# Kernel tuning notes

Measured on AMD Instinct MI355X. Metric: run time of the kernel, lower is better.

Reference implementation:

```python
import jax, jax.numpy as jnp
import numpy as np

B, S, D, F, E, NS, K = 2, 1024, 1024, 4096, 8, 8, 2
FS = F // NS  # shared-expert hidden size = d_ff // num_shared_experts


def setup_inputs() -> dict:
    key = jax.random.key(0)
    ks = jax.random.split(key, 8)
    scale = 0.02
    return {
        "hidden_states": jax.random.normal(ks[0], (B, S, D), jnp.float32),
        "gate_W": jax.random.normal(ks[1], (E, D), jnp.float32) * scale,
        "w1_e": jax.random.normal(ks[2], (E, D, F), jnp.float32) * scale,
        "w3_e": jax.random.normal(ks[3], (E, D, F), jnp.float32) * scale,
        "w2_e": jax.random.normal(ks[4], (E, F, D), jnp.float32) * scale,
        "w1_s": jax.random.normal(ks[5], (NS, D, FS), jnp.float32) * scale,
        "w3_s": jax.random.normal(ks[6], (NS, D, FS), jnp.float32) * scale,
        "w2_s": jax.random.normal(ks[7], (NS, FS, D), jnp.float32) * scale,
    }


def reference(hidden_states, gate_W, w1_e, w3_e, w2_e, w1_s, w3_s, w2_s):
    b, s, d = hidden_states.shape
    e = gate_W.shape[0]
    flat = hidden_states.reshape(-1, d)            # [T, D]
    T = flat.shape[0]

    # --- gate: softmax over experts, top-k probs scattered (k=0 slot only survives) ---
    logits = (flat @ gate_W.T).astype(jnp.float32)  # [T, E]
    probs = jax.nn.softmax(logits, axis=-1)
    top_v, top_i = jax.lax.top_k(probs, K)          # [T, K]
    gates = jnp.zeros((T, e), probs.dtype).at[jnp.arange(T)[:, None], top_i].set(top_v)

    # --- routed experts: module runs every expert densely on all tokens ---
    g = jax.nn.silu(jnp.einsum('td,edf->etf', flat, w1_e))  # [E, T, F]
    u = jnp.einsum('td,edf->etf', flat, w3_e)
    out_e = jnp.einsum('etf,efd->etd', g * u, w2_e)         # [E, T, D]
    routed = jnp.einsum('te,etd->td', gates, out_e).reshape(b, s, d)

    # --- shared experts (mean over NS experts) ---
    gs = jax.nn.silu(jnp.einsum('bsd,ndf->nbsf', hidden_states, w1_s))
    us = jnp.einsum('bsd,ndf->nbsf', hidden_states, w3_s)
    shared = jnp.einsum('nbsf,nfd->bsd', gs * us, w2_s) / w1_s.shape[0]

    alpha = 0.5
    return alpha * shared + (1.0 - alpha) * routed
```

## Files before the change

kernel.cpp:

```cpp
#include <hip/hip_runtime.h>

#define T 2048
#define D 1024
#define F 4096
#define E 8
#define NS 8
#define FS 512
#define SHB 5120
#define NROWS 7168
#define MT_MAX 56

typedef float floatx4 __attribute__((ext_vector_type(4)));
typedef short short8 __attribute__((ext_vector_type(8)));

__device__ __forceinline__ unsigned short f2bf(float f) {
  unsigned int u = __float_as_uint(f);
  u += 0x7FFF + ((u >> 16) & 1);
  return (unsigned short)(u >> 16);
}

__device__ __forceinline__ void glds16(const void* g, void* l) {
  __builtin_amdgcn_global_load_lds(
      (const __attribute__((address_space(1))) void*)g,
      (__attribute__((address_space(3))) void*)l, 16, 0, 0);
}

__global__ void gate_kernel(const float* __restrict__ x, const float* __restrict__ gW,
                            unsigned short* __restrict__ xb, int* __restrict__ cnt,
                            int* __restrict__ list_tok, float* __restrict__ list_gate) {
  int t = blockIdx.x, tid = threadIdx.x;
  const float* xr = x + (size_t)t * D;
  float acc[E];
#pragma unroll
  for (int e = 0; e < E; ++e) acc[e] = 0.f;
  for (int d = tid; d < D; d += 256) {
    float xv = xr[d];
    xb[(size_t)t * D + d] = f2bf(xv);
#pragma unroll
    for (int e = 0; e < E; ++e) acc[e] += xv * gW[e * D + d];
  }
#pragma unroll
  for (int o = 32; o > 0; o >>= 1)
#pragma unroll
    for (int e = 0; e < E; ++e) acc[e] += __shfl_down(acc[e], o, 64);
  __shared__ float wred[4][E];
  int lane = tid & 63, wv = tid >> 6;
  if (lane == 0)
#pragma unroll
    for (int e = 0; e < E; ++e) wred[wv][e] = acc[e];
  __syncthreads();
  if (tid == 0) {
    float l[E];
#pragma unroll
    for (int e = 0; e < E; ++e) l[e] = wred[0][e] + wred[1][e] + wred[2][e] + wred[3][e];
    int i1 = 0; float m1 = l[0];
    for (int e = 1; e < E; ++e) if (l[e] > m1) { m1 = l[e]; i1 = e; }
    int i2 = -1; float m2 = -3.4e38f;
    for (int e = 0; e < E; ++e) if (e != i1 && l[e] > m2) { m2 = l[e]; i2 = e; }
    float s = 0.f, p[E];
#pragma unroll
    for (int e = 0; e < E; ++e) { p[e] = __expf(l[e] - m1); s += p[e]; }
    float inv = 1.f / s;
    int p1 = atomicAdd(&cnt[i1], 1);
    list_tok[i1 * T + p1] = t; list_gate[i1 * T + p1] = p[i1] * inv;
    int p2 = atomicAdd(&cnt[i2], 1);
    list_tok[i2 * T + p2] = t; list_gate[i2 * T + p2] = p[i2] * inv;
  }
}

__global__ void offsets_kernel(const int* __restrict__ cnt, int* __restrict__ off,
                               int* __restrict__ mt_expert) {
  if (threadIdx.x == 0 && blockIdx.x == 0) {
    int o = 0;
    for (int e = 0; e < E; ++e) { off[e] = o; o += (cnt[e] + 127) & ~127; }
    off[E] = o;
    for (int i = 0; i < MT_MAX; ++i) mt_expert[i] = -1;
    for (int e = 0; e < E; ++e) {
      int t0 = off[e] >> 7, nt = (cnt[e] + 127) >> 7;
      for (int i = 0; i < nt; ++i) mt_expert[t0 + i] = e;
    }
    for (int i = SHB >> 7; i < MT_MAX; ++i) mt_expert[i] = E;
  }
}

__global__ void scatter_kernel(const int* __restrict__ cnt, const int* __restrict__ off,
                               const int* __restrict__ list_tok, const float* __restrict__ list_gate,
                               int* __restrict__ tok_of_row, float* __restrict__ row_scale,
                               int* __restrict__ tok_rows, int* __restrict__ tk) {
  int idx = blockIdx.x * 256 + threadIdx.x;
  int e = idx >> 11, i = idx & (T - 1);
  if (e < E && i < cnt[e]) {
    int row = off[e] + i;
    int t = list_tok[e * T + i];
    tok_of_row[row] = t;
    row_scale[row] = 0.5f * list_gate[e * T + i];
    int k = atomicAdd(&tk[t], 1);
    tok_rows[2 * t + k] = row;
  }
}

__global__ void transpose_cast(const float* __restrict__ in, unsigned short* __restrict__ out,
                               int R, int C) {
  in += (size_t)blockIdx.z * R * C;
  out += (size_t)blockIdx.z * R * C;
  int r0 = blockIdx.y * 32, c0 = blockIdx.x * 32;
  __shared__ float tile[32][33];
  int tid = threadIdx.x;
  {
    int rl = tid >> 3, cl = (tid & 7) * 4;
    float4 v = *(const float4*)(in + (size_t)(r0 + rl) * C + c0 + cl);
    tile[rl][cl] = v.x; tile[rl][cl + 1] = v.y;
    tile[rl][cl + 2] = v.z; tile[rl][cl + 3] = v.w;
  }
  __syncthreads();
  {
    int cl = tid >> 3, rq = (tid & 7) * 4;
    int c = c0 + cl, r = r0 + rq;
    ushort4 v;
    v.x = f2bf(tile[rq][cl]);     v.y = f2bf(tile[rq + 1][cl]);
    v.z = f2bf(tile[rq + 2][cl]); v.w = f2bf(tile[rq + 3][cl]);
    int Rt = R >> 5;
    size_t o = ((size_t)(c >> 7) * Rt + (r >> 5)) * 4096 + (size_t)(c & 127) * 32 + (r & 31);
    *(ushort4*)(out + o) = v;
  }
}

__global__ __launch_bounds__(256, 2) void up_gemm(
    const unsigned short* __restrict__ xb, const unsigned short* __restrict__ W1T,
    const unsigned short* __restrict__ W3T, const unsigned short* __restrict__ W1sT,
    const unsigned short* __restrict__ W3sT, const int* __restrict__ mt_expert,
    const int* __restrict__ tok_of_row, unsigned short* __restrict__ Hb) {
  int mt = blockIdx.y, ntile = blockIdx.x;
  int e = mt_expert[mt];
  if (e < 0) return;
  const unsigned short *B1, *B3;
  if (e < E) {
    B1 = W1T + (size_t)e * F * D;
    B3 = W3T + (size_t)e * F * D;
  } else {
    B1 = W1sT; B3 = W3sT;
  }
  __shared__ unsigned short Au0[128 * 32], B1u0[128 * 32], B3u0[128 * 32];
  __shared__ unsigned short Au1[128 * 32], B1u1[128 * 32], B3u1[128 * 32];
  __shared__ unsigned short Au2[128 * 32], B1u2[128 * 32], B3u2[128 * 32];
  int tid = threadIdx.x;
  int lane = tid & 63, wv = tid >> 6, wm = wv >> 1, wn = wv & 1;
  int row16 = lane & 15, quad = lane >> 4;
  int qsw8 = (quad ^ ((lane >> 1) & 3)) * 8;
  int swzb = (tid >> 2) * 64 + (((tid & 3) ^ ((tid >> 3) & 3)) * 16);
  int lw = wv * 1024;

  int r1 = tid >> 2;
  int hrow1 = mt * 128 + r1, hrow2 = hrow1 + 64;
  int srow1 = (e < E) ? tok_of_row[hrow1] : (hrow1 - SHB);
  int srow2 = (e < E) ? tok_of_row[hrow2] : (hrow2 - SHB);
  int asl = ((tid & 3) ^ ((tid >> 3) & 3)) * 16;
  const char* asrc1 = (const char*)(xb + (size_t)srow1 * D) + asl;
  const char* asrc2 = (const char*)(xb + (size_t)srow2 * D) + asl;
  const char* b1t = (const char*)(B1 + (size_t)ntile * (D / 32) * 4096);
  const char* b3t = (const char*)(B3 + (size_t)ntile * (D / 32) * 4096);

  floatx4 accg[4][4], accu[4][4];
#pragma unroll
  for (int i = 0; i < 4; ++i)
#pragma unroll
    for (int j = 0; j < 4; ++j) {
      accg[i][j] = (floatx4){0.f, 0.f, 0.f, 0.f};
      accu[i][j] = (floatx4){0.f, 0.f, 0.f, 0.f};
    }

  auto stage = [&](int kt, unsigned short* Ad, unsigned short* B1d, unsigned short* B3d) {
    size_t ko = (size_t)kt * 64;
    size_t bo = (size_t)kt * 8192;
    glds16(asrc1 + ko, (char*)Ad + lw);
    glds16(asrc2 + ko, (char*)Ad + 4096 + lw);
    glds16(b1t + bo + swzb, (char*)B1d + lw);
    glds16(b1t + bo + 4096 + swzb, (char*)B1d + 4096 + lw);
    glds16(b3t + bo + swzb, (char*)B3d + lw);
    glds16(b3t + bo + 4096 + swzb, (char*)B3d + 4096 + lw);
  };
  auto compute = [&](const unsigned short* Ac, const unsigned short* B1c,
                     const unsigned short* B3c) {
    short8 af[4], b1f[4], b3f[4];
#pragma unroll
    for (int mi = 0; mi < 4; ++mi)
      af[mi] = *(const short8*)(Ac + (wm * 64 + mi * 16 + row16) * 32 + qsw8);
#pragma unroll
    for (int ni = 0; ni < 4; ++ni) {
      b1f[ni] = *(const short8*)(B1c + (wn * 64 + ni * 16 + row16) * 32 + qsw8);
      b3f[ni] = *(const short8*)(B3c + (wn * 64 + ni * 16 + row16) * 32 + qsw8);
    }
#pragma unroll
    for (int mi = 0; mi < 4; ++mi)
#pragma unroll
      for (int ni = 0; ni < 4; ++ni) {
        accg[mi][ni] = __builtin_amdgcn_mfma_f32_16x16x32_bf16(af[mi], b1f[ni], accg[mi][ni], 0, 0, 0);
        accu[mi][ni] = __builtin_amdgcn_mfma_f32_16x16x32_bf16(af[mi], b3f[ni], accu[mi][ni], 0, 0, 0);
      }
  };

  stage(0, Au0, B1u0, B3u0);
  stage(1, Au1, B1u1, B3u1);
  asm volatile("s_waitcnt vmcnt(6)" ::: "memory");
  __builtin_amdgcn_s_barrier();
  for (int t = 0; t < 30; t += 3) {
    stage(t + 2, Au2, B1u2, B3u2);
    compute(Au0, B1u0, B3u0);
    asm volatile("s_waitcnt vmcnt(6)" ::: "memory");
    __builtin_amdgcn_s_barrier();
    stage(t + 3, Au0, B1u0, B3u0);
    compute(Au1, B1u1, B3u1);
    asm volatile("s_waitcnt vmcnt(6)" ::: "memory");
    __builtin_amdgcn_s_barrier();
    stage(t + 4, Au1, B1u1, B3u1);
    compute(Au2, B1u2, B3u2);
    asm volatile("s_waitcnt vmcnt(6)" ::: "memory");
    __builtin_amdgcn_s_barrier();
  }
  compute(Au0, B1u0, B3u0);
  asm volatile("s_waitcnt vmcnt(0)" ::: "memory");
  __builtin_amdgcn_s_barrier();
  compute(Au1, B1u1, B3u1);

#pragma unroll
  for (int mi = 0; mi < 4; ++mi)
#pragma unroll
    for (int ni = 0; ni < 4; ++ni)
#pragma unroll
      for (int r = 0; r < 4; ++r) {
        int hrow = mt * 128 + wm * 64 + mi * 16 + quad * 4 + r;
        int col = ntile * 128 + wn * 64 + ni * 16 + row16;
        float g = accg[mi][ni][r], u = accu[mi][ni][r];
        float h = g * u / (1.0f + __expf(-g));
        size_t o = ((size_t)(hrow >> 7) * 128 + (col >> 5)) * 4096 + (size_t)(hrow & 127) * 32 + (col & 31);
        Hb[o] = f2bf(h);
      }
}

__global__ __launch_bounds__(256, 2) void down_gemm(
    const unsigned short* __restrict__ Hb, const unsigned short* __restrict__ W2T,
    const unsigned short* __restrict__ W2sT, const int* __restrict__ mt_expert,
    const float* __restrict__ row_scale, float* __restrict__ O) {
  int mt = blockIdx.y, ntile = blockIdx.x, kz = blockIdx.z;
  int e = mt_expert[mt];
  if (e < 0) return;
  const char* Bt = (const char*)(((e < E) ? (W2T + (size_t)e * D * F) : W2sT)
                                 + (size_t)ntile * (F / 32) * 4096);
  const char* At = (const char*)(Hb + (size_t)mt * (F / 32) * 4096);
  O += (size_t)kz * NROWS * D;
  __shared__ unsigned short Ad0[128 * 32], Bd0[128 * 32];
  __shared__ unsigned short Ad1[128 * 32], Bd1[128 * 32];
  __shared__ unsigned short Ad2[128 * 32], Bd2[128 * 32];
  int tid = threadIdx.x;
  int lane = tid & 63, wv = tid >> 6, wm = wv >> 1, wn = wv & 1;
  int row16 = lane & 15, quad = lane >> 4;
  int qsw8 = (quad ^ ((lane >> 1) & 3)) * 8;
  int swzb = (tid >> 2) * 64 + (((tid & 3) ^ ((tid >> 3) & 3)) * 16);
  int lw = wv * 1024;
  floatx4 acc[4][4];
#pragma unroll
  for (int i = 0; i < 4; ++i)
#pragma unroll
    for (int j = 0; j < 4; ++j) acc[i][j] = (floatx4){0.f, 0.f, 0.f, 0.f};

  auto stage = [&](int kt, unsigned short* Ad, unsigned short* Bd) {
    size_t o = (size_t)kt * 8192;
    glds16(At + o + swzb, (char*)Ad + lw);
    glds16(At + o + 4096 + swzb, (char*)Ad + 4096 + lw);
    glds16(Bt + o + swzb, (char*)Bd + lw);
    glds16(Bt + o + 4096 + swzb, (char*)Bd + 4096 + lw);
  };
  auto compute = [&](const unsigned short* Ac, const unsigned short* Bc) {
    short8 af[4], bf[4];
#pragma unroll
    for (int mi = 0; mi < 4; ++mi)
      af[mi] = *(const short8*)(Ac + (wm * 64 + mi * 16 + row16) * 32 + qsw8);
#pragma unroll
    for (int ni = 0; ni < 4; ++ni)
      bf[ni] = *(const short8*)(Bc + (wn * 64 + ni * 16 + row16) * 32 + qsw8);
#pragma unroll
    for (int mi = 0; mi < 4; ++mi)
#pragma unroll
      for (int ni = 0; ni < 4; ++ni)
        acc[mi][ni] = __builtin_amdgcn_mfma_f32_16x16x32_bf16(af[mi], bf[ni], acc[mi][ni], 0, 0, 0);
  };

  int k0 = kz * 64;
  stage(k0 + 0, Ad0, Bd0);
  stage(k0 + 1, Ad1, Bd1);
  asm volatile("s_waitcnt vmcnt(4)" ::: "memory");
  __builtin_amdgcn_s_barrier();
  for (int t = 0; t < 60; t += 3) {
    stage(k0 + t + 2, Ad2, Bd2);
    compute(Ad0, Bd0);
    asm volatile("s_waitcnt vmcnt(4)" ::: "memory");
    __builtin_amdgcn_s_barrier();
    stage(k0 + t + 3, Ad0, Bd0);
    compute(Ad1, Bd1);
    asm volatile("s_waitcnt vmcnt(4)" ::: "memory");
    __builtin_amdgcn_s_barrier();
    stage(k0 + t + 4, Ad1, Bd1);
    compute(Ad2, Bd2);
    asm volatile("s_waitcnt vmcnt(4)" ::: "memory");
    __builtin_amdgcn_s_barrier();
  }
  stage(k0 + 62, Ad2, Bd2);
  compute(Ad0, Bd0);
  asm volatile("s_waitcnt vmcnt(4)" ::: "memory");
  __builtin_amdgcn_s_barrier();
  stage(k0 + 63, Ad0, Bd0);
  compute(Ad1, Bd1);
  asm volatile("s_waitcnt vmcnt(4)" ::: "memory");
  __builtin_amdgcn_s_barrier();
  compute(Ad2, Bd2);
  asm volatile("s_waitcnt vmcnt(0)" ::: "memory");
  __builtin_amdgcn_s_barrier();
  compute(Ad0, Bd0);

#pragma unroll
  for (int mi = 0; mi < 4; ++mi)
#pragma unroll
    for (int ni = 0; ni < 4; ++ni)
#pragma unroll
      for (int r = 0; r < 4; ++r) {
        int grow = mt * 128 + wm * 64 + mi * 16 + quad * 4 + r;
        int col = ntile * 128 + wn * 64 + ni * 16 + row16;
        float scale = (grow < SHB) ? row_scale[grow] : 0.0625f;
        O[(size_t)grow * D + col] = acc[mi][ni][r] * scale;
      }
}

__global__ void combine_kernel(const float* __restrict__ O, const int* __restrict__ tok_rows,
                               float* __restrict__ out) {
  int idx = blockIdx.x * 256 + threadIdx.x;
  int t = idx >> 8, c = idx & 255;
  int r0 = tok_rows[2 * t], r1 = tok_rows[2 * t + 1];
  const float4* O4 = (const float4*)O;
  const size_t HLF = (size_t)NROWS * 256;
  float4 a = O4[(size_t)r0 * 256 + c];
  float4 b = O4[(size_t)r1 * 256 + c];
  float4 s = O4[((size_t)SHB + t) * 256 + c];
  float4 a2 = O4[HLF + (size_t)r0 * 256 + c];
  float4 b2 = O4[HLF + (size_t)r1 * 256 + c];
  float4 s2 = O4[HLF + ((size_t)SHB + t) * 256 + c];
  float4 r;
  r.x = a.x + b.x + s.x + a2.x + b2.x + s2.x;
  r.y = a.y + b.y + s.y + a2.y + b2.y + s2.y;
  r.z = a.z + b.z + s.z + a2.z + b2.z + s2.z;
  r.w = a.w + b.w + s.w + a2.w + b2.w + s2.w;
  ((float4*)out)[idx] = r;
}

extern "C" void kernel_launch(void* const* d_in, const int* in_sizes, int n_in,
                              void* d_out, int out_size, void* d_ws, size_t ws_size,
                              hipStream_t stream) {
  (void)in_sizes; (void)n_in; (void)out_size; (void)ws_size;
  const float* x   = (const float*)d_in[0];
  const float* gW  = (const float*)d_in[1];
  const float* w1e = (const float*)d_in[2];
  const float* w3e = (const float*)d_in[3];
  const float* w2e = (const float*)d_in[4];
  const float* w1s = (const float*)d_in[5];
  const float* w3s = (const float*)d_in[6];
  const float* w2s = (const float*)d_in[7];
  float* out = (float*)d_out;

  char* w = (char*)d_ws;
  auto alloc = [&](size_t bytes) {
    char* p = w; w += (bytes + 255) & ~(size_t)255; return p;
  };
  unsigned short* xb   = (unsigned short*)alloc((size_t)T * D * 2);
  unsigned short* W1T  = (unsigned short*)alloc((size_t)E * F * D * 2);
  unsigned short* W3T  = (unsigned short*)alloc((size_t)E * F * D * 2);
  unsigned short* W2T  = (unsigned short*)alloc((size_t)E * D * F * 2);
  unsigned short* W1sT = (unsigned short*)alloc((size_t)F * D * 2);
  unsigned short* W3sT = (unsigned short*)alloc((size_t)F * D * 2);
  unsigned short* W2sT = (unsigned short*)alloc((size_t)D * F * 2);
  unsigned short* Hb   = (unsigned short*)alloc((size_t)NROWS * F * 2);
  float* Ob        = (float*)alloc((size_t)2 * NROWS * D * 4);
  float* row_scale = (float*)alloc((size_t)SHB * 4);
  float* list_gate = (float*)alloc((size_t)E * T * 4);
  int* list_tok    = (int*)alloc((size_t)E * T * 4);
  int* tok_rows    = (int*)alloc((size_t)T * 2 * 4);
  int* offv        = (int*)alloc(16 * 4);
  int* mt_expert   = (int*)alloc(64 * 4);
  int* ctrl        = (int*)alloc((size_t)(8 + T + SHB) * 4);
  int* cnt = ctrl; int* tk = ctrl + 8; int* tok_of_row = ctrl + 8 + T;

  hipMemsetAsync(ctrl, 0, (size_t)(8 + T + SHB) * 4, stream);
  gate_kernel<<<T, 256, 0, stream>>>(x, gW, xb, cnt, list_tok, list_gate);
  offsets_kernel<<<1, 64, 0, stream>>>(cnt, offv, mt_expert);
  scatter_kernel<<<(E * T) / 256, 256, 0, stream>>>(cnt, offv, list_tok, list_gate,
                                                    tok_of_row, row_scale, tok_rows, tk);
  transpose_cast<<<dim3(F / 32, D / 32, E), 256, 0, stream>>>(w1e, W1T, D, F);
  transpose_cast<<<dim3(F / 32, D / 32, E), 256, 0, stream>>>(w3e, W3T, D, F);
  transpose_cast<<<dim3(D / 32, F / 32, E), 256, 0, stream>>>(w2e, W2T, F, D);
  transpose_cast<<<dim3(FS / 32, D / 32, NS), 256, 0, stream>>>(w1s, W1sT, D, FS);
  transpose_cast<<<dim3(FS / 32, D / 32, NS), 256, 0, stream>>>(w3s, W3sT, D, FS);
  transpose_cast<<<dim3(D / 32, F / 32, 1), 256, 0, stream>>>(w2s, W2sT, F, D);
  up_gemm<<<dim3(F / 128, MT_MAX), 256, 0, stream>>>(xb, W1T, W3T, W1sT, W3sT,
                                                     mt_expert, tok_of_row, Hb);
  down_gemm<<<dim3(D / 128, MT_MAX, 2), 256, 0, stream>>>(Hb, W2T, W2sT, mt_expert, row_scale, Ob);
  combine_kernel<<<(T * D / 4) / 256, 256, 0, stream>>>(Ob, tok_rows, out);
}
```

Baseline: 721.9 us.

## Enlarge transpose tiles, pair w1/w3 casts, and drop down-GEMM split-K

The weight transpose-cast now uses 64x64 tiles with 8-wide bf16 stores, and the w1/w3 transposes share one launch each. The down GEMM stops splitting K into two halves, so it writes a single fp32 output buffer and the combine kernel reads three rows per token instead of six. The gate kernel is vectorized with float4 loads. The aim is less HBM traffic for the partial outputs, fewer launches and wider memory accesses. The cost is half as many down-GEMM blocks, which lowers parallelism, and a longer serial K loop per block.

```diff
diff --git a/kernel.cpp b/kernel.cpp
--- a/kernel.cpp
+++ b/kernel.cpp
@@ -12,6 +12,7 @@
 
 typedef float floatx4 __attribute__((ext_vector_type(4)));
 typedef short short8 __attribute__((ext_vector_type(8)));
+typedef unsigned short ushort8v __attribute__((ext_vector_type(8)));
 
 __device__ __forceinline__ unsigned short f2bf(float f) {
   unsigned int u = __float_as_uint(f);
@@ -29,15 +30,17 @@
                             unsigned short* __restrict__ xb, int* __restrict__ cnt,
                             int* __restrict__ list_tok, float* __restrict__ list_gate) {
   int t = blockIdx.x, tid = threadIdx.x;
-  const float* xr = x + (size_t)t * D;
+  const float4* xr = (const float4*)(x + (size_t)t * D);
+  const float4* g4 = (const float4*)gW;
+  float4 xv = xr[tid];
+  ushort4 xo;
+  xo.x = f2bf(xv.x); xo.y = f2bf(xv.y); xo.z = f2bf(xv.z); xo.w = f2bf(xv.w);
+  *(ushort4*)(xb + (size_t)t * D + tid * 4) = xo;
   float acc[E];
 #pragma unroll
-  for (int e = 0; e < E; ++e) acc[e] = 0.f;
-  for (int d = tid; d < D; d += 256) {
-    float xv = xr[d];
-    xb[(size_t)t * D + d] = f2bf(xv);
-#pragma unroll
-    for (int e = 0; e < E; ++e) acc[e] += xv * gW[e * D + d];
+  for (int e = 0; e < E; ++e) {
+    float4 w = g4[e * 256 + tid];
+    acc[e] = xv.x * w.x + xv.y * w.y + xv.z * w.z + xv.w * w.w;
   }
 #pragma unroll
   for (int o = 32; o > 0; o >>= 1)
@@ -99,30 +102,55 @@
   }
 }
 
+__device__ __forceinline__ void tc64(const float* __restrict__ in,
+                                     unsigned short* __restrict__ out, int R, int C) {
+  int r0 = blockIdx.y * 64, c0 = blockIdx.x * 64;
+  __shared__ float tile[64][65];
+  int tid = threadIdx.x;
+  {
+    int cl4 = (tid & 15) * 4;
+    int rl0 = tid >> 4;
+#pragma unroll
+    for (int k = 0; k < 4; ++k) {
+      int rl = rl0 + k * 16;
+      float4 v = *(const float4*)(in + (size_t)(r0 + rl) * C + c0 + cl4);
+      tile[rl][cl4] = v.x; tile[rl][cl4 + 1] = v.y;
+      tile[rl][cl4 + 2] = v.z; tile[rl][cl4 + 3] = v.w;
+    }
+  }
+  __syncthreads();
+  {
+    int cl = tid >> 2;
+    int rq = tid & 3;
+    int c = c0 + cl;
+    int Rt = R >> 5;
+    size_t cbase = ((size_t)(c >> 7) * Rt) * 4096 + (size_t)(c & 127) * 32;
+#pragma unroll
+    for (int s = 0; s < 2; ++s) {
+      int rr = s * 32 + rq * 8;
+      int r = r0 + rr;
+      ushort8v v;
+#pragma unroll
+      for (int j = 0; j < 8; ++j) v[j] = f2bf(tile[rr + j][cl]);
+      size_t o = cbase + (size_t)(r >> 5) * 4096 + (r & 31);
+      *(ushort8v*)(out + o) = v;
+    }
+  }
+}
+
 __global__ void transpose_cast(const float* __restrict__ in, unsigned short* __restrict__ out,
                                int R, int C) {
-  in += (size_t)blockIdx.z * R * C;
-  out += (size_t)blockIdx.z * R * C;
-  int r0 = blockIdx.y * 32, c0 = blockIdx.x * 32;
-  __shared__ float tile[32][33];
-  int tid = threadIdx.x;
-  {
-    int rl = tid >> 3, cl = (tid & 7) * 4;
-    float4 v = *(const float4*)(in + (size_t)(r0 + rl) * C + c0 + cl);
-    tile[rl][cl] = v.x; tile[rl][cl + 1] = v.y;
-    tile[rl][cl + 2] = v.z; tile[rl][cl + 3] = v.w;
-  }
-  __syncthreads();
-  {
-    int cl = tid >> 3, rq = (tid & 7) * 4;
-    int c = c0 + cl, r = r0 + rq;
-    ushort4 v;
-    v.x = f2bf(tile[rq][cl]);     v.y = f2bf(tile[rq + 1][cl]);
-    v.z = f2bf(tile[rq + 2][cl]); v.w = f2bf(tile[rq + 3][cl]);
-    int Rt = R >> 5;
-    size_t o = ((size_t)(c >> 7) * Rt + (r >> 5)) * 4096 + (size_t)(c & 127) * 32 + (r & 31);
-    *(ushort4*)(out + o) = v;
-  }
+  tc64(in + (size_t)blockIdx.z * R * C, out + (size_t)blockIdx.z * R * C, R, C);
+}
+
+__global__ void transpose_cast_pair(const float* __restrict__ inA, const float* __restrict__ inB,
+                                    unsigned short* __restrict__ outA,
+                                    unsigned short* __restrict__ outB, int R, int C) {
+  int z = blockIdx.z, h = gridDim.z >> 1;
+  const float* in = (z < h) ? inA : inB;
+  unsigned short* out = (z < h) ? outA : outB;
+  int zz = (z < h) ? z : z - h;
+  tc64(in + (size_t)zz * R * C, out + (size_t)zz * R * C, R, C);
 }
 
 __global__ __launch_bounds__(256, 2) void up_gemm(
@@ -241,13 +269,12 @@
     const unsigned short* __restrict__ Hb, const unsigned short* __restrict__ W2T,
     const unsigned short* __restrict__ W2sT, const int* __restrict__ mt_expert,
     const float* __restrict__ row_scale, float* __restrict__ O) {
-  int mt = blockIdx.y, ntile = blockIdx.x, kz = blockIdx.z;
+  int mt = blockIdx.y, ntile = blockIdx.x;
   int e = mt_expert[mt];
   if (e < 0) return;
   const char* Bt = (const char*)(((e < E) ? (W2T + (size_t)e * D * F) : W2sT)
                                  + (size_t)ntile * (F / 32) * 4096);
   const char* At = (const char*)(Hb + (size_t)mt * (F / 32) * 4096);
-  O += (size_t)kz * NROWS * D;
   __shared__ unsigned short Ad0[128 * 32], Bd0[128 * 32];
   __shared__ unsigned short Ad1[128 * 32], Bd1[128 * 32];
   __shared__ unsigned short Ad2[128 * 32], Bd2[128 * 32];
@@ -285,37 +312,28 @@
         acc[mi][ni] = __builtin_amdgcn_mfma_f32_16x16x32_bf16(af[mi], bf[ni], acc[mi][ni], 0, 0, 0);
   };
 
-  int k0 = kz * 64;
-  stage(k0 + 0, Ad0, Bd0);
-  stage(k0 + 1, Ad1, Bd1);
+  stage(0, Ad0, Bd0);
+  stage(1, Ad1, Bd1);
   asm volatile("s_waitcnt vmcnt(4)" ::: "memory");
   __builtin_amdgcn_s_barrier();
-  for (int t = 0; t < 60; t += 3) {
-    stage(k0 + t + 2, Ad2, Bd2);
+  for (int t = 0; t < 126; t += 3) {
+    stage(t + 2, Ad2, Bd2);
     compute(Ad0, Bd0);
     asm volatile("s_waitcnt vmcnt(4)" ::: "memory");
     __builtin_amdgcn_s_barrier();
-    stage(k0 + t + 3, Ad0, Bd0);
+    stage(t + 3, Ad0, Bd0);
     compute(Ad1, Bd1);
     asm volatile("s_waitcnt vmcnt(4)" ::: "memory");
     __builtin_amdgcn_s_barrier();
-    stage(k0 + t + 4, Ad1, Bd1);
+    stage(t + 4, Ad1, Bd1);
     compute(Ad2, Bd2);
     asm volatile("s_waitcnt vmcnt(4)" ::: "memory");
     __builtin_amdgcn_s_barrier();
   }
-  stage(k0 + 62, Ad2, Bd2);
   compute(Ad0, Bd0);
-  asm volatile("s_waitcnt vmcnt(4)" ::: "memory");
-  __builtin_amdgcn_s_barrier();
-  stage(k0 + 63, Ad0, Bd0);
-  compute(Ad1, Bd1);
-  asm volatile("s_waitcnt vmcnt(4)" ::: "memory");
-  __builtin_amdgcn_s_barrier();
-  compute(Ad2, Bd2);
   asm volatile("s_waitcnt vmcnt(0)" ::: "memory");
   __builtin_amdgcn_s_barrier();
-  compute(Ad0, Bd0);
+  compute(Ad1, Bd1);
 
 #pragma unroll
   for (int mi = 0; mi < 4; ++mi)
@@ -336,18 +354,14 @@
   int t = idx >> 8, c = idx & 255;
   int r0 = tok_rows[2 * t], r1 = tok_rows[2 * t + 1];
   const float4* O4 = (const float4*)O;
-  const size_t HLF = (size_t)NROWS * 256;
   float4 a = O4[(size_t)r0 * 256 + c];
   float4 b = O4[(size_t)r1 * 256 + c];
   float4 s = O4[((size_t)SHB + t) * 256 + c];
-  float4 a2 = O4[HLF + (size_t)r0 * 256 + c];
-  float4 b2 = O4[HLF + (size_t)r1 * 256 + c];
-  float4 s2 = O4[HLF + ((size_t)SHB + t) * 256 + c];
   float4 r;
-  r.x = a.x + b.x + s.x + a2.x + b2.x + s2.x;
-  r.y = a.y + b.y + s.y + a2.y + b2.y + s2.y;
-  r.z = a.z + b.z + s.z + a2.z + b2.z + s2.z;
-  r.w = a.w + b.w + s.w + a2.w + b2.w + s2.w;
+  r.x = a.x + b.x + s.x;
+  r.y = a.y + b.y + s.y;
+  r.z = a.z + b.z + s.z;
+  r.w = a.w + b.w + s.w;
   ((float4*)out)[idx] = r;
 }
 
@@ -377,7 +391,7 @@
   unsigned short* W3sT = (unsigned short*)alloc((size_t)F * D * 2);
   unsigned short* W2sT = (unsigned short*)alloc((size_t)D * F * 2);
   unsigned short* Hb   = (unsigned short*)alloc((size_t)NROWS * F * 2);
-  float* Ob        = (float*)alloc((size_t)2 * NROWS * D * 4);
+  float* Ob        = (float*)alloc((size_t)NROWS * D * 4);
   float* row_scale = (float*)alloc((size_t)SHB * 4);
   float* list_gate = (float*)alloc((size_t)E * T * 4);
   int* list_tok    = (int*)alloc((size_t)E * T * 4);
@@ -392,14 +406,12 @@
   offsets_kernel<<<1, 64, 0, stream>>>(cnt, offv, mt_expert);
   scatter_kernel<<<(E * T) / 256, 256, 0, stream>>>(cnt, offv, list_tok, list_gate,
                                                     tok_of_row, row_scale, tok_rows, tk);
-  transpose_cast<<<dim3(F / 32, D / 32, E), 256, 0, stream>>>(w1e, W1T, D, F);
-  transpose_cast<<<dim3(F / 32, D / 32, E), 256, 0, stream>>>(w3e, W3T, D, F);
-  transpose_cast<<<dim3(D / 32, F / 32, E), 256, 0, stream>>>(w2e, W2T, F, D);
-  transpose_cast<<<dim3(FS / 32, D / 32, NS), 256, 0, stream>>>(w1s, W1sT, D, FS);
-  transpose_cast<<<dim3(FS / 32, D / 32, NS), 256, 0, stream>>>(w3s, W3sT, D, FS);
-  transpose_cast<<<dim3(D / 32, F / 32, 1), 256, 0, stream>>>(w2s, W2sT, F, D);
+  transpose_cast_pair<<<dim3(F / 64, D / 64, 2 * E), 256, 0, stream>>>(w1e, w3e, W1T, W3T, D, F);
+  transpose_cast<<<dim3(D / 64, F / 64, E), 256, 0, stream>>>(w2e, W2T, F, D);
+  transpose_cast_pair<<<dim3(FS / 64, D / 64, 2 * NS), 256, 0, stream>>>(w1s, w3s, W1sT, W3sT, D, FS);
+  transpose_cast<<<dim3(D / 64, F / 64, 1), 256, 0, stream>>>(w2s, W2sT, F, D);
   up_gemm<<<dim3(F / 128, MT_MAX), 256, 0, stream>>>(xb, W1T, W3T, W1sT, W3sT,
                                                      mt_expert, tok_of_row, Hb);
-  down_gemm<<<dim3(D / 128, MT_MAX, 2), 256, 0, stream>>>(Hb, W2T, W2sT, mt_expert, row_scale, Ob);
+  down_gemm<<<dim3(D / 128, MT_MAX), 256, 0, stream>>>(Hb, W2T, W2sT, mt_expert, row_scale, Ob);
   combine_kernel<<<(T * D / 4) / 256, 256, 0, stream>>>(Ob, tok_rows, out);
 }
```

Result: faster. 698.3 us (-3.3%).
